# Kernel optimization log

Measured on AMD Instinct MI355X. Metric: run time of the kernel, lower is better.

Reference implementation:

```python
import jax, jax.numpy as jnp
import numpy as np

L, H, E, T, B, V = 8, 16, 1024, 1024, 2, 800
D = E // H  # head_size = 64
STD = 0.02


def setup_inputs() -> dict:
    key = jax.random.key(0)
    ks = iter(jax.random.split(key, 32))

    def nrm(shape):
        return jax.random.normal(next(ks), shape, jnp.float32) * STD

    latlong = jax.random.uniform(next(ks), (B, T, 2), jnp.float32)
    wl = jax.random.uniform(next(ks), (B, T, 1), jnp.float32, minval=3.0, maxval=11.0)
    inp = {
        "idx": jnp.concatenate([latlong, wl], axis=-1),  # [B,T,3]
        "tok_table": nrm((V, E)),
        "pos_W": nrm((2, E)),
        "pos_b": jnp.zeros((E,), jnp.float32),
        # stacked per-layer params (per-head q/k/v linears fused into [E,E])
        "Wq": nrm((L, E, E)),
        "Wk": nrm((L, E, E)),
        "Wv": nrm((L, E, E)),
        "Wo": nrm((L, E, E)),
        "bo": jnp.zeros((L, E), jnp.float32),
        "W1": nrm((L, E, 4 * E)),
        "b1": jnp.zeros((L, 4 * E), jnp.float32),
        "W2": nrm((L, 4 * E, E)),
        "b2": jnp.zeros((L, E), jnp.float32),
        "ln1_g": jnp.ones((L, E), jnp.float32),
        "ln1_b": jnp.zeros((L, E), jnp.float32),
        "ln2_g": jnp.ones((L, E), jnp.float32),
        "ln2_b": jnp.zeros((L, E), jnp.float32),
        "lnf_g": jnp.ones((E,), jnp.float32),
        "lnf_b": jnp.zeros((E,), jnp.float32),
        "lm_W": nrm((E, V)),
        "lm_b": jnp.zeros((V,), jnp.float32),
    }
    return inp


def _ln(x, g, b, eps=1e-5):
    m = x.mean(-1, keepdims=True)
    v = x.var(-1, keepdims=True)
    return (x - m) * jax.lax.rsqrt(v + eps) * g + b


def _block(x, p):
    Wq, Wk, Wv, Wo, bo, W1, b1, W2, b2, g1, be1, g2, be2 = p
    Bx, Tx, _ = x.shape
    h = _ln(x, g1, be1)
    q = (h @ Wq).reshape(Bx, Tx, H, D)
    k = (h @ Wk).reshape(Bx, Tx, H, D)
    v = (h @ Wv).reshape(Bx, Tx, H, D)
    scores = jnp.einsum('bqhd,bkhd->bhqk', q, k) * (D ** -0.5)
    mask = jnp.tril(jnp.ones((Tx, Tx), bool))  # causal
    scores = jnp.where(mask, scores, -jnp.inf)
    w = jax.nn.softmax(scores, axis=-1)  # dropout=0 (eval) -> identity
    attn = jnp.einsum('bhqk,bkhd->bqhd', w, v).reshape(Bx, Tx, E)
    x = x + attn @ Wo + bo
    h = _ln(x, g2, be2)
    x = x + jax.nn.relu(h @ W1 + b1) @ W2 + b2
    return x


def reference(idx, tok_table, pos_W, pos_b, Wq, Wk, Wv, Wo, bo, W1, b1, W2, b2,
              ln1_g, ln1_b, ln2_g, ln2_b, lnf_g, lnf_b, lm_W, lm_b):
    # water level channel -> token id in [0, V-1]
    idx_wl = jnp.clip(jnp.round(idx[..., 2] * 100.0 - 300.0), 0, V - 1).astype(jnp.int32)
    tok_emb = tok_table[idx_wl]                      # [B,T,E]
    pos_emb = idx[..., :2] @ pos_W + pos_b           # [B,T,E]
    x = tok_emb + pos_emb

    params = (Wq, Wk, Wv, Wo, bo, W1, b1, W2, b2, ln1_g, ln1_b, ln2_g, ln2_b)

    def body(carry, p):
        return _block(carry, p), None

    x, _ = jax.lax.scan(body, x, params)
    x = _ln(x, lnf_g, lnf_b)
    logits = x @ lm_W + lm_b                         # [B,T,V]
    return logits
```

## Files before the change

kernel.cpp:

```cpp
#include <hip/hip_runtime.h>
#include <hip/hip_bf16.h>

#define L_ 8
#define H_ 16
#define E_ 1024
#define T_ 1024
#define B_ 2
#define V_ 800
#define D_ 64
#define FF_ 4096
#define N_ (B_ * T_)
#define QS_ 3072

typedef unsigned short u16;
typedef __bf16 bf16x8 __attribute__((ext_vector_type(8)));
typedef float f32x4 __attribute__((ext_vector_type(4)));

__device__ __forceinline__ u16 f2b(float f) {
    unsigned int u = __float_as_uint(f);
    unsigned int r = (u + 0x7fffu + ((u >> 16) & 1u)) >> 16;
    return (u16)r;
}

__device__ __forceinline__ void gld16(const u16* g, u16* l) {
    __builtin_amdgcn_global_load_lds(
        (__attribute__((address_space(1))) void*)(uintptr_t)g,
        (__attribute__((address_space(3))) void*)(unsigned)(uintptr_t)l,
        16, 0, 0);
}

__global__ __launch_bounds__(256) void embed_k(
    const float* __restrict__ idx, const float* __restrict__ tok,
    const float* __restrict__ posW, const float* __restrict__ posb,
    float* __restrict__ x)
{
    int row = blockIdx.x;
    int e = threadIdx.x * 4;
    float lat = idx[row * 3 + 0];
    float lon = idx[row * 3 + 1];
    float wl  = idx[row * 3 + 2];
    float tf = rintf(wl * 100.0f - 300.0f);
    tf = fminf(fmaxf(tf, 0.0f), (float)(V_ - 1));
    int tkn = (int)tf;

    float4 tv = *(const float4*)(tok + (size_t)tkn * E_ + e);
    float4 p0 = *(const float4*)(posW + e);
    float4 p1 = *(const float4*)(posW + E_ + e);
    float4 pb = *(const float4*)(posb + e);
    float4 ov;
    ov.x = tv.x + lat * p0.x + lon * p1.x + pb.x;
    ov.y = tv.y + lat * p0.y + lon * p1.y + pb.y;
    ov.z = tv.z + lat * p0.z + lon * p1.z + pb.z;
    ov.w = tv.w + lat * p0.w + lon * p1.w + pb.w;
    *(float4*)(x + (size_t)row * E_ + e) = ov;
}

__global__ __launch_bounds__(256) void ln_k(
    const float* __restrict__ x, const float* __restrict__ g,
    const float* __restrict__ bta, u16* __restrict__ out)
{
    __shared__ float rs[4], rq[4];
    int row = blockIdx.x;
    int tid = threadIdx.x;
    const float* xr = x + (size_t)row * E_;
    float4 xv = *(const float4*)(xr + tid * 4);
    float s = xv.x + xv.y + xv.z + xv.w;
    float q = xv.x * xv.x + xv.y * xv.y + xv.z * xv.z + xv.w * xv.w;
    #pragma unroll
    for (int off = 32; off; off >>= 1) {
        s += __shfl_xor(s, off, 64);
        q += __shfl_xor(q, off, 64);
    }
    int wv = tid >> 6, ln = tid & 63;
    if (ln == 0) { rs[wv] = s; rq[wv] = q; }
    __syncthreads();
    s = rs[0] + rs[1] + rs[2] + rs[3];
    q = rq[0] + rq[1] + rq[2] + rq[3];
    float mean = s * (1.0f / E_);
    float var  = q * (1.0f / E_) - mean * mean;
    float inv  = 1.0f / sqrtf(var + 1e-5f);
    int c = tid * 4;
    float4 gv = *(const float4*)(g + c);
    float4 bv = *(const float4*)(bta + c);
    ushort4 ov;
    ov.x = f2b((xv.x - mean) * inv * gv.x + bv.x);
    ov.y = f2b((xv.y - mean) * inv * gv.y + bv.y);
    ov.z = f2b((xv.z - mean) * inv * gv.z + bv.z);
    ov.w = f2b((xv.w - mean) * inv * gv.w + bv.w);
    *(ushort4*)(out + (size_t)row * E_ + c) = ov;
}

__global__ __launch_bounds__(256) void comb_ln_k(
    const float* __restrict__ Cp, const float* __restrict__ bias,
    float* __restrict__ x, const float* __restrict__ g,
    const float* __restrict__ bta, u16* __restrict__ hout)
{
    __shared__ float rs[4], rq[4];
    int row = blockIdx.x;
    int tid = threadIdx.x;
    int c = tid * 4;
    size_t off = (size_t)row * E_ + c;
    const size_t total = (size_t)N_ * E_;
    float4 p0 = *(const float4*)(Cp + off);
    float4 p1 = *(const float4*)(Cp + total + off);
    float4 xv = *(const float4*)(x + off);
    float4 bv = *(const float4*)(bias + c);
    xv.x += p0.x + p1.x + bv.x;
    xv.y += p0.y + p1.y + bv.y;
    xv.z += p0.z + p1.z + bv.z;
    xv.w += p0.w + p1.w + bv.w;
    *(float4*)(x + off) = xv;

    float s = xv.x + xv.y + xv.z + xv.w;
    float q = xv.x * xv.x + xv.y * xv.y + xv.z * xv.z + xv.w * xv.w;
    #pragma unroll
    for (int o = 32; o; o >>= 1) {
        s += __shfl_xor(s, o, 64);
        q += __shfl_xor(q, o, 64);
    }
    int wv = tid >> 6, ln = tid & 63;
    if (ln == 0) { rs[wv] = s; rq[wv] = q; }
    __syncthreads();
    s = rs[0] + rs[1] + rs[2] + rs[3];
    q = rq[0] + rq[1] + rq[2] + rq[3];
    float mean = s * (1.0f / E_);
    float var  = q * (1.0f / E_) - mean * mean;
    float inv  = 1.0f / sqrtf(var + 1e-5f);
    float4 gv = *(const float4*)(g + c);
    float4 bb = *(const float4*)(bta + c);
    ushort4 ov;
    ov.x = f2b((xv.x - mean) * inv * gv.x + bb.x);
    ov.y = f2b((xv.y - mean) * inv * gv.y + bb.y);
    ov.z = f2b((xv.z - mean) * inv * gv.z + bb.z);
    ov.w = f2b((xv.w - mean) * inv * gv.w + bb.w);
    *(ushort4*)(hout + off) = ov;
}

__device__ __forceinline__ void wtrans_body(
    const float* __restrict__ W, u16* __restrict__ Wt, int K, int M,
    int m0, int k0)
{
    __shared__ float tile[64][65];
    int tid = threadIdx.x;
    int rr = tid >> 4, c4 = (tid & 15) * 4;
    if (m0 + 64 <= M) {
        #pragma unroll
        for (int p = 0; p < 4; p++) {
            int kk = rr + p * 16;
            float4 v4 = *(const float4*)(W + (size_t)(k0 + kk) * M + m0 + c4);
            tile[kk][c4 + 0] = v4.x; tile[kk][c4 + 1] = v4.y;
            tile[kk][c4 + 2] = v4.z; tile[kk][c4 + 3] = v4.w;
        }
    } else {
        #pragma unroll
        for (int p = 0; p < 4; p++) {
            int kk = rr + p * 16;
            const float* wr = W + (size_t)(k0 + kk) * M;
            #pragma unroll
            for (int c = 0; c < 4; c++) {
                int m = m0 + c4 + c;
                tile[kk][c4 + c] = (m < M) ? wr[m] : 0.0f;
            }
        }
    }
    __syncthreads();
    #pragma unroll
    for (int p = 0; p < 4; p++) {
        int ml = rr + p * 16;
        ushort4 o;
        o.x = f2b(tile[c4 + 0][ml]);
        o.y = f2b(tile[c4 + 1][ml]);
        o.z = f2b(tile[c4 + 2][ml]);
        o.w = f2b(tile[c4 + 3][ml]);
        *(ushort4*)(Wt + (size_t)(m0 + ml) * K + k0 + c4) = o;
    }
}

__global__ __launch_bounds__(256) void wtrans_k(
    const float* __restrict__ W, u16* __restrict__ Wt, int K, int M)
{
    wtrans_body(W, Wt, K, M, blockIdx.x * 64, blockIdx.y * 64);
}

__global__ __launch_bounds__(256) void wtrans_all_k(
    const float* __restrict__ Wq, const float* __restrict__ Wk,
    const float* __restrict__ Wv, const float* __restrict__ Wo,
    const float* __restrict__ W1, const float* __restrict__ W2,
    u16* __restrict__ wqkv_t, u16* __restrict__ wo_t,
    u16* __restrict__ w1_t, u16* __restrict__ w2_t)
{
    int bx = blockIdx.x, by = blockIdx.y, z = blockIdx.z;
    const size_t M1 = 1024 * 1024;
    if (z < 4) {
        if (bx >= 16) return;
        const float* W = (z == 0) ? Wq : (z == 1) ? Wk : (z == 2) ? Wv : Wo;
        u16* dst = (z < 3) ? (wqkv_t + (size_t)z * M1) : wo_t;
        wtrans_body(W, dst, E_, E_, bx * 64, by * 64);
    } else if (z == 4) {
        wtrans_body(W1, w1_t, E_, FF_, bx * 64, by * 64);
    } else {
        int id = by * 64 + bx;
        int mb = id >> 6, kb = id & 63;
        wtrans_body(W2, w2_t, FF_, E_, mb * 64, kb * 64);
    }
}

__global__ __launch_bounds__(256) void gemm_bf16(
    const u16* __restrict__ A, const u16* __restrict__ Bt,
    const float* __restrict__ bias, const float* __restrict__ res,
    float* __restrict__ Cf, u16* __restrict__ Cb, float* __restrict__ Cp,
    int K, int M, int relu)
{
    __shared__ __align__(16) u16 As[128 * 32];
    __shared__ __align__(16) u16 Bs[128 * 32];
    int tid = threadIdx.x;
    int bm = blockIdx.y * 128, bn = blockIdx.x * 128;
    int zz = blockIdx.z;
    int kslice = K / (int)gridDim.z;
    int lane = tid & 63, wv = tid >> 6;
    int l15 = lane & 15, q4 = lane >> 4;
    int wm = (wv & 1) * 64, wn = (wv >> 1) * 64;

    const u16* ga = A + (size_t)(bm + (tid >> 2)) * K + zz * kslice + (tid & 3) * 8;
    const u16* gb = Bt + (size_t)(bn + (tid >> 2)) * K + zz * kslice + (tid & 3) * 8;
    size_t gstep = (size_t)64 * K;
    u16* lA0 = As + wv * (16 * 32);
    u16* lB0 = Bs + wv * (16 * 32);

    f32x4 acc[4][4];
    #pragma unroll
    for (int i = 0; i < 4; i++)
        #pragma unroll
        for (int j = 0; j < 4; j++)
            acc[i][j] = (f32x4){0.0f, 0.0f, 0.0f, 0.0f};

    for (int k0 = 0; k0 < kslice; k0 += 32) {
        gld16(ga, lA0);
        gld16(ga + gstep, lA0 + 64 * 32);
        gld16(gb, lB0);
        gld16(gb + gstep, lB0 + 64 * 32);
        ga += 32; gb += 32;
        __syncthreads();

        const bf16x8* Ap = (const bf16x8*)As + (wm + l15) * 4 + q4;
        const bf16x8* Bp = (const bf16x8*)Bs + (wn + l15) * 4 + q4;
        bf16x8 af[4], bg[4];
        #pragma unroll
        for (int i = 0; i < 4; i++) { af[i] = Ap[i * 64]; bg[i] = Bp[i * 64]; }
        #pragma unroll
        for (int i = 0; i < 4; i++)
            #pragma unroll
            for (int j = 0; j < 4; j++)
                acc[i][j] = __builtin_amdgcn_mfma_f32_16x16x32_bf16(
                    af[i], bg[j], acc[i][j], 0, 0, 0);
        __syncthreads();
    }

    size_t poff = (size_t)zz * N_ * M;
    #pragma unroll
    for (int i = 0; i < 4; i++) {
        int r0 = bm + wm + i * 16 + q4 * 4;
        #pragma unroll
        for (int j = 0; j < 4; j++) {
            int col = bn + wn + j * 16 + l15;
            if (col < M) {
                if (Cp) {
                    #pragma unroll
                    for (int r = 0; r < 4; r++)
                        Cp[poff + (size_t)(r0 + r) * M + col] = acc[i][j][r];
                } else {
                    float bv = bias ? bias[col] : 0.0f;
                    #pragma unroll
                    for (int r = 0; r < 4; r++) {
                        size_t off = (size_t)(r0 + r) * M + col;
                        float v = acc[i][j][r] + bv;
                        if (res) v += res[off];
                        if (relu) v = fmaxf(v, 0.0f);
                        if (Cb) Cb[off] = f2b(v); else Cf[off] = v;
                    }
                }
            }
        }
    }
}

__global__ __launch_bounds__(256) void combine_k(
    const float* __restrict__ Cp, const float* __restrict__ bias,
    float* __restrict__ Cf, int M, int total)
{
    int e = (blockIdx.x * 256 + threadIdx.x) * 4;
    if (e >= total) return;
    float4 a = *(const float4*)(Cp + e);
    float4 b = *(const float4*)(Cp + (size_t)total + e);
    a.x += b.x; a.y += b.y; a.z += b.z; a.w += b.w;
    int col = e % M;
    if (bias) {
        float4 bv = *(const float4*)(bias + col);
        a.x += bv.x; a.y += bv.y; a.z += bv.z; a.w += bv.w;
    }
    *(float4*)(Cf + e) = a;
}

__global__ __launch_bounds__(256) void vtrans_k(
    const u16* __restrict__ QKV, u16* __restrict__ Vt)
{
    __shared__ u16 tile[64][72];
    int t0 = blockIdx.x * 64, h = blockIdx.y, b = blockIdx.z;
    int tid = threadIdx.x;
    int row = tid >> 3, c8 = (tid & 7) * 8;
    #pragma unroll
    for (int p = 0; p < 2; p++) {
        int t = row + p * 32;
        *(float4*)&tile[t][c8] = *(const float4*)(
            QKV + (size_t)(b * T_ + t0 + t) * QS_ + 2 * E_ + h * D_ + c8);
    }
    __syncthreads();
    #pragma unroll
    for (int p = 0; p < 2; p++) {
        int d = row + p * 32;
        u16 o[8];
        #pragma unroll
        for (int j = 0; j < 8; j++) o[j] = tile[c8 + j][d];
        *(ushort4*)(Vt + ((size_t)(b * H_ + h) * D_ + d) * T_ + t0 + c8) =
            *(ushort4*)&o[0];
        *(ushort4*)(Vt + ((size_t)(b * H_ + h) * D_ + d) * T_ + t0 + c8 + 4) =
            *(ushort4*)&o[4];
    }
}

__global__ __launch_bounds__(256) void attn_mfma_k(
    const u16* __restrict__ QKV, const u16* __restrict__ Vt,
    u16* __restrict__ O)
{
    __shared__ __align__(16) u16 Ps[4][16 * 72];
    int tid = threadIdx.x;
    int wv = tid >> 6, lane = tid & 63;
    int c = lane & 15, q4 = lane >> 4;
    int qb = (int)(gridDim.x - 1) - (int)blockIdx.x;
    int h = blockIdx.y, b = blockIdx.z;
    int q0 = qb * 64 + wv * 16;
    const float scale = 0.125f;

    const u16* qrow = QKV + (size_t)(b * T_ + q0 + c) * QS_ + h * D_;
    bf16x8 qf0 = *(const bf16x8*)(qrow + q4 * 8);
    bf16x8 qf1 = *(const bf16x8*)(qrow + 32 + q4 * 8);

    const u16* kbase  = QKV + (size_t)b * T_ * QS_ + E_ + h * D_;
    const u16* vtbase = Vt + (size_t)(b * H_ + h) * D_ * T_;

    float l_acc[4] = {0.0f, 0.0f, 0.0f, 0.0f};
    f32x4 acc_o[4];
    #pragma unroll
    for (int nt = 0; nt < 4; nt++) acc_o[nt] = (f32x4){0.f, 0.f, 0.f, 0.f};

    u16* ps = &Ps[wv][0];

    for (int kt = 0; kt <= qb; kt++) {
        int k0 = kt * 64;
        bool diag = (kt == qb);

        bf16x8 kf[4][2];
        #pragma unroll
        for (int j = 0; j < 4; j++) {
            const u16* kr = kbase + (size_t)(k0 + 16 * j + c) * QS_ + q4 * 8;
            kf[j][0] = *(const bf16x8*)(kr);
            kf[j][1] = *(const bf16x8*)(kr + 32);
        }

        #pragma unroll
        for (int j = 0; j < 4; j++) {
            f32x4 sa = (f32x4){0.f, 0.f, 0.f, 0.f};
            sa = __builtin_amdgcn_mfma_f32_16x16x32_bf16(qf0, kf[j][0], sa, 0, 0, 0);
            sa = __builtin_amdgcn_mfma_f32_16x16x32_bf16(qf1, kf[j][1], sa, 0, 0, 0);
            #pragma unroll
            for (int r = 0; r < 4; r++) {
                bool masked = diag && (k0 + 16 * j + c > q0 + 4 * q4 + r);
                float pj = masked ? 0.0f : __expf(sa[r] * scale);
                l_acc[r] += pj;
                ps[(4 * q4 + r) * 72 + 16 * j + c] = f2b(pj);
            }
        }
        bf16x8 pf0 = *(const bf16x8*)(ps + c * 72 + q4 * 8);
        bf16x8 pf1 = *(const bf16x8*)(ps + c * 72 + 32 + q4 * 8);

        bf16x8 vf[4][2];
        #pragma unroll
        for (int nt = 0; nt < 4; nt++) {
            const u16* vr = vtbase + (size_t)(16 * nt + c) * T_ + k0 + q4 * 8;
            vf[nt][0] = *(const bf16x8*)(vr);
            vf[nt][1] = *(const bf16x8*)(vr + 32);
        }

        #pragma unroll
        for (int nt = 0; nt < 4; nt++) {
            acc_o[nt] = __builtin_amdgcn_mfma_f32_16x16x32_bf16(pf0, vf[nt][0], acc_o[nt], 0, 0, 0);
            acc_o[nt] = __builtin_amdgcn_mfma_f32_16x16x32_bf16(pf1, vf[nt][1], acc_o[nt], 0, 0, 0);
        }
    }

    #pragma unroll
    for (int r = 0; r < 4; r++) {
        float ts = l_acc[r];
        ts += __shfl_xor(ts, 1, 64);
        ts += __shfl_xor(ts, 2, 64);
        ts += __shfl_xor(ts, 4, 64);
        ts += __shfl_xor(ts, 8, 64);
        l_acc[r] = ts;
    }

    #pragma unroll
    for (int r = 0; r < 4; r++) {
        float inv = 1.0f / l_acc[r];
        size_t orow = (size_t)(b * T_ + q0 + 4 * q4 + r) * E_ + h * D_;
        #pragma unroll
        for (int nt = 0; nt < 4; nt++)
            O[orow + 16 * nt + c] = f2b(acc_o[nt][r] * inv);
    }
}

extern "C" void kernel_launch(void* const* d_in, const int* in_sizes, int n_in,
                              void* d_out, int out_size, void* d_ws, size_t ws_size,
                              hipStream_t stream)
{
    const float* idx   = (const float*)d_in[0];
    const float* tok   = (const float*)d_in[1];
    const float* posW  = (const float*)d_in[2];
    const float* posb  = (const float*)d_in[3];
    const float* Wq    = (const float*)d_in[4];
    const float* Wk    = (const float*)d_in[5];
    const float* Wv    = (const float*)d_in[6];
    const float* Wo    = (const float*)d_in[7];
    const float* bo    = (const float*)d_in[8];
    const float* W1    = (const float*)d_in[9];
    const float* b1    = (const float*)d_in[10];
    const float* W2    = (const float*)d_in[11];
    const float* b2    = (const float*)d_in[12];
    const float* ln1g  = (const float*)d_in[13];
    const float* ln1b  = (const float*)d_in[14];
    const float* ln2g  = (const float*)d_in[15];
    const float* ln2b  = (const float*)d_in[16];
    const float* lnfg  = (const float*)d_in[17];
    const float* lnfb  = (const float*)d_in[18];
    const float* lmW   = (const float*)d_in[19];
    const float* lmb   = (const float*)d_in[20];
    float* out = (float*)d_out;

    const size_t M1 = 1024 * 1024;
    float* ws    = (float*)d_ws;
    float* x     = ws;
    float* cpart = x + 2 * M1;
    u16* qkv   = (u16*)(cpart + 4 * M1);
    u16* vt    = qkv + 6 * M1;
    u16* h_bf  = vt + 2 * M1;
    u16* ao_bf = h_bf + 2 * M1;
    u16* ff_bf = ao_bf + 2 * M1;
    u16* wq_t  = ff_bf + 8 * M1;
    u16* wo_t  = wq_t + 3 * M1;
    u16* w1_t  = wo_t + 1 * M1;
    u16* w2_t  = w1_t + 4 * M1;
    u16* wlm_t = w2_t + 4 * M1;

    dim3 blk(256);
    dim3 gQKV(3072 / 128, N_ / 128, 1);
    dim3 gWo(1024 / 128, N_ / 128, 2);
    dim3 gW1(4096 / 128, N_ / 128, 1);
    dim3 gW2(1024 / 128, N_ / 128, 2);
    dim3 gLM(7, N_ / 128, 2);
    dim3 gAT(T_ / 64, H_, B_);
    dim3 gWT(64, 16, 6);
    dim3 tLM(14, 16);
    int totLM = N_ * V_;
    dim3 cLM(totLM / 4 / 256);

    embed_k<<<N_, blk, 0, stream>>>(idx, tok, posW, posb, x);
    ln_k<<<N_, blk, 0, stream>>>(x, ln1g, ln1b, h_bf);

    for (int l = 0; l < L_; l++) {
        size_t oEE = (size_t)l * E_ * E_;
        size_t oE  = (size_t)l * E_;
        size_t oEF = (size_t)l * E_ * FF_;
        size_t oF  = (size_t)l * FF_;

        wtrans_all_k<<<gWT, blk, 0, stream>>>(
            Wq + oEE, Wk + oEE, Wv + oEE, Wo + oEE, W1 + oEF, W2 + oEF,
            wq_t, wo_t, w1_t, w2_t);
        gemm_bf16<<<gQKV, blk, 0, stream>>>(h_bf, wq_t, nullptr, nullptr,
                                            nullptr, qkv, nullptr, E_, QS_, 0);
        vtrans_k<<<gAT, blk, 0, stream>>>(qkv, vt);
        attn_mfma_k<<<gAT, blk, 0, stream>>>(qkv, vt, ao_bf);
        gemm_bf16<<<gWo, blk, 0, stream>>>(ao_bf, wo_t, nullptr, nullptr,
                                           nullptr, nullptr, cpart, E_, E_, 0);
        comb_ln_k<<<N_, blk, 0, stream>>>(cpart, bo + oE, x,
                                          ln2g + oE, ln2b + oE, h_bf);
        gemm_bf16<<<gW1, blk, 0, stream>>>(h_bf, w1_t, b1 + oF, nullptr,
                                           nullptr, ff_bf, nullptr, E_, FF_, 1);
        gemm_bf16<<<gW2, blk, 0, stream>>>(ff_bf, w2_t, nullptr, nullptr,
                                           nullptr, nullptr, cpart, FF_, E_, 0);
        if (l < L_ - 1) {
            comb_ln_k<<<N_, blk, 0, stream>>>(cpart, b2 + oE, x,
                                              ln1g + oE + E_, ln1b + oE + E_, h_bf);
        } else {
            comb_ln_k<<<N_, blk, 0, stream>>>(cpart, b2 + oE, x,
                                              lnfg, lnfb, h_bf);
        }
    }

    wtrans_k<<<tLM, blk, 0, stream>>>(lmW, wlm_t, E_, V_);
    gemm_bf16<<<gLM, blk, 0, stream>>>(h_bf, wlm_t, nullptr, nullptr,
                                       nullptr, nullptr, cpart, E_, V_, 0);
    combine_k<<<cLM, blk, 0, stream>>>(cpart, lmb, out, V_, totLM);
}
```

Before: 2.172 ms.

## Hoist weight transposes, fuse V-transpose into QKV GEMM, fuse embed+LN, deepen W2 split-K

```diff
diff --git a/kernel.cpp b/kernel.cpp
--- a/kernel.cpp
+++ b/kernel.cpp
@@ -29,13 +29,16 @@
         16, 0, 0);
 }
 
-__global__ __launch_bounds__(256) void embed_k(
+__global__ __launch_bounds__(256) void embed_ln_k(
     const float* __restrict__ idx, const float* __restrict__ tok,
     const float* __restrict__ posW, const float* __restrict__ posb,
-    float* __restrict__ x)
-{
+    const float* __restrict__ g, const float* __restrict__ bta,
+    float* __restrict__ x, u16* __restrict__ hout)
+{
+    __shared__ float rs[4], rq[4];
     int row = blockIdx.x;
-    int e = threadIdx.x * 4;
+    int tid = threadIdx.x;
+    int e = tid * 4;
     float lat = idx[row * 3 + 0];
     float lon = idx[row * 3 + 1];
     float wl  = idx[row * 3 + 2];
@@ -47,23 +50,13 @@
     float4 p0 = *(const float4*)(posW + e);
     float4 p1 = *(const float4*)(posW + E_ + e);
     float4 pb = *(const float4*)(posb + e);
-    float4 ov;
-    ov.x = tv.x + lat * p0.x + lon * p1.x + pb.x;
-    ov.y = tv.y + lat * p0.y + lon * p1.y + pb.y;
-    ov.z = tv.z + lat * p0.z + lon * p1.z + pb.z;
-    ov.w = tv.w + lat * p0.w + lon * p1.w + pb.w;
-    *(float4*)(x + (size_t)row * E_ + e) = ov;
-}
-
-__global__ __launch_bounds__(256) void ln_k(
-    const float* __restrict__ x, const float* __restrict__ g,
-    const float* __restrict__ bta, u16* __restrict__ out)
-{
-    __shared__ float rs[4], rq[4];
-    int row = blockIdx.x;
-    int tid = threadIdx.x;
-    const float* xr = x + (size_t)row * E_;
-    float4 xv = *(const float4*)(xr + tid * 4);
+    float4 xv;
+    xv.x = tv.x + lat * p0.x + lon * p1.x + pb.x;
+    xv.y = tv.y + lat * p0.y + lon * p1.y + pb.y;
+    xv.z = tv.z + lat * p0.z + lon * p1.z + pb.z;
+    xv.w = tv.w + lat * p0.w + lon * p1.w + pb.w;
+    *(float4*)(x + (size_t)row * E_ + e) = xv;
+
     float s = xv.x + xv.y + xv.z + xv.w;
     float q = xv.x * xv.x + xv.y * xv.y + xv.z * xv.z + xv.w * xv.w;
     #pragma unroll
@@ -79,19 +72,18 @@
     float mean = s * (1.0f / E_);
     float var  = q * (1.0f / E_) - mean * mean;
     float inv  = 1.0f / sqrtf(var + 1e-5f);
-    int c = tid * 4;
-    float4 gv = *(const float4*)(g + c);
-    float4 bv = *(const float4*)(bta + c);
+    float4 gv = *(const float4*)(g + e);
+    float4 bb = *(const float4*)(bta + e);
     ushort4 ov;
-    ov.x = f2b((xv.x - mean) * inv * gv.x + bv.x);
-    ov.y = f2b((xv.y - mean) * inv * gv.y + bv.y);
-    ov.z = f2b((xv.z - mean) * inv * gv.z + bv.z);
-    ov.w = f2b((xv.w - mean) * inv * gv.w + bv.w);
-    *(ushort4*)(out + (size_t)row * E_ + c) = ov;
+    ov.x = f2b((xv.x - mean) * inv * gv.x + bb.x);
+    ov.y = f2b((xv.y - mean) * inv * gv.y + bb.y);
+    ov.z = f2b((xv.z - mean) * inv * gv.z + bb.z);
+    ov.w = f2b((xv.w - mean) * inv * gv.w + bb.w);
+    *(ushort4*)(hout + (size_t)row * E_ + e) = ov;
 }
 
 __global__ __launch_bounds__(256) void comb_ln_k(
-    const float* __restrict__ Cp, const float* __restrict__ bias,
+    const float* __restrict__ Cp, int ns, const float* __restrict__ bias,
     float* __restrict__ x, const float* __restrict__ g,
     const float* __restrict__ bta, u16* __restrict__ hout)
 {
@@ -101,14 +93,13 @@
     int c = tid * 4;
     size_t off = (size_t)row * E_ + c;
     const size_t total = (size_t)N_ * E_;
-    float4 p0 = *(const float4*)(Cp + off);
-    float4 p1 = *(const float4*)(Cp + total + off);
     float4 xv = *(const float4*)(x + off);
     float4 bv = *(const float4*)(bias + c);
-    xv.x += p0.x + p1.x + bv.x;
-    xv.y += p0.y + p1.y + bv.y;
-    xv.z += p0.z + p1.z + bv.z;
-    xv.w += p0.w + p1.w + bv.w;
+    xv.x += bv.x; xv.y += bv.y; xv.z += bv.z; xv.w += bv.w;
+    for (int s2 = 0; s2 < ns; s2++) {
+        float4 p = *(const float4*)(Cp + (size_t)s2 * total + off);
+        xv.x += p.x; xv.y += p.y; xv.z += p.z; xv.w += p.w;
+    }
     *(float4*)(x + off) = xv;
 
     float s = xv.x + xv.y + xv.z + xv.w;
@@ -186,22 +177,50 @@
     const float* __restrict__ Wq, const float* __restrict__ Wk,
     const float* __restrict__ Wv, const float* __restrict__ Wo,
     const float* __restrict__ W1, const float* __restrict__ W2,
-    u16* __restrict__ wqkv_t, u16* __restrict__ wo_t,
-    u16* __restrict__ w1_t, u16* __restrict__ w2_t)
-{
+    u16* __restrict__ wt)
+{
+    const size_t MU = 1024 * 1024;
     int bx = blockIdx.x, by = blockIdx.y, z = blockIdx.z;
-    const size_t M1 = 1024 * 1024;
     if (z < 4) {
         if (bx >= 16) return;
         const float* W = (z == 0) ? Wq : (z == 1) ? Wk : (z == 2) ? Wv : Wo;
-        u16* dst = (z < 3) ? (wqkv_t + (size_t)z * M1) : wo_t;
-        wtrans_body(W, dst, E_, E_, bx * 64, by * 64);
+        wtrans_body(W, wt + (size_t)z * MU, E_, E_, bx * 64, by * 64);
     } else if (z == 4) {
-        wtrans_body(W1, w1_t, E_, FF_, bx * 64, by * 64);
+        wtrans_body(W1, wt + 4 * MU, E_, FF_, bx * 64, by * 64);
     } else {
         int id = by * 64 + bx;
-        int mb = id >> 6, kb = id & 63;
-        wtrans_body(W2, w2_t, FF_, E_, mb * 64, kb * 64);
+        wtrans_body(W2, wt + 8 * MU, FF_, E_, (id >> 6) * 64, (id & 63) * 64);
+    }
+}
+
+__global__ __launch_bounds__(256) void wtrans_hoist_k(
+    const float* __restrict__ Wq, const float* __restrict__ Wk,
+    const float* __restrict__ Wv, const float* __restrict__ Wo,
+    const float* __restrict__ W1, const float* __restrict__ W2,
+    const float* __restrict__ lmW,
+    u16* __restrict__ wslab, u16* __restrict__ wlm)
+{
+    const size_t MU = 1024 * 1024;
+    int bx = blockIdx.x, by = blockIdx.y, z = blockIdx.z;
+    if (z == 48) {
+        if (bx >= 14) return;
+        wtrans_body(lmW, wlm, E_, V_, bx * 64, by * 64);
+        return;
+    }
+    int l = z / 6, m = z % 6;
+    u16* wt = wslab + (size_t)l * 12 * MU;
+    size_t oEE = (size_t)l * E_ * E_;
+    size_t oEF = (size_t)l * E_ * FF_;
+    if (m < 4) {
+        if (bx >= 16) return;
+        const float* W = (m == 0) ? Wq + oEE : (m == 1) ? Wk + oEE
+                       : (m == 2) ? Wv + oEE : Wo + oEE;
+        wtrans_body(W, wt + (size_t)m * MU, E_, E_, bx * 64, by * 64);
+    } else if (m == 4) {
+        wtrans_body(W1 + oEF, wt + 4 * MU, E_, FF_, bx * 64, by * 64);
+    } else {
+        int id = by * 64 + bx;
+        wtrans_body(W2 + oEF, wt + 8 * MU, FF_, E_, (id >> 6) * 64, (id & 63) * 64);
     }
 }
 
@@ -209,7 +228,7 @@
     const u16* __restrict__ A, const u16* __restrict__ Bt,
     const float* __restrict__ bias, const float* __restrict__ res,
     float* __restrict__ Cf, u16* __restrict__ Cb, float* __restrict__ Cp,
-    int K, int M, int relu)
+    u16* __restrict__ vtout, int K, int M, int relu)
 {
     __shared__ __align__(16) u16 As[128 * 32];
     __shared__ __align__(16) u16 Bs[128 * 32];
@@ -276,7 +295,17 @@
                         float v = acc[i][j][r] + bv;
                         if (res) v += res[off];
                         if (relu) v = fmaxf(v, 0.0f);
-                        if (Cb) Cb[off] = f2b(v); else Cf[off] = v;
+                        if (vtout && col >= 2 * E_) {
+                            int dd = col - 2 * E_;
+                            int hh = dd >> 6, dl = dd & 63;
+                            int rowi = r0 + r;
+                            int bb = rowi >> 10, tt = rowi & 1023;
+                            vtout[((size_t)(bb * H_ + hh) * D_ + dl) * T_ + tt] = f2b(v);
+                        } else if (Cb) {
+                            Cb[off] = f2b(v);
+                        } else {
+                            Cf[off] = v;
+                        }
                     }
                 }
             }
@@ -299,33 +328,6 @@
         a.x += bv.x; a.y += bv.y; a.z += bv.z; a.w += bv.w;
     }
     *(float4*)(Cf + e) = a;
-}
-
-__global__ __launch_bounds__(256) void vtrans_k(
-    const u16* __restrict__ QKV, u16* __restrict__ Vt)
-{
-    __shared__ u16 tile[64][72];
-    int t0 = blockIdx.x * 64, h = blockIdx.y, b = blockIdx.z;
-    int tid = threadIdx.x;
-    int row = tid >> 3, c8 = (tid & 7) * 8;
-    #pragma unroll
-    for (int p = 0; p < 2; p++) {
-        int t = row + p * 32;
-        *(float4*)&tile[t][c8] = *(const float4*)(
-            QKV + (size_t)(b * T_ + t0 + t) * QS_ + 2 * E_ + h * D_ + c8);
-    }
-    __syncthreads();
-    #pragma unroll
-    for (int p = 0; p < 2; p++) {
-        int d = row + p * 32;
-        u16 o[8];
-        #pragma unroll
-        for (int j = 0; j < 8; j++) o[j] = tile[c8 + j][d];
-        *(ushort4*)(Vt + ((size_t)(b * H_ + h) * D_ + d) * T_ + t0 + c8) =
-            *(ushort4*)&o[0];
-        *(ushort4*)(Vt + ((size_t)(b * H_ + h) * D_ + d) * T_ + t0 + c8 + 4) =
-            *(ushort4*)&o[4];
-    }
 }
 
 __global__ __launch_bounds__(256) void attn_mfma_k(
@@ -445,35 +447,45 @@
     const float* lmb   = (const float*)d_in[20];
     float* out = (float*)d_out;
 
-    const size_t M1 = 1024 * 1024;
+    const size_t MU = 1024ull * 1024ull;
+    size_t need_big = (2 + 8) * MU * 4
+                    + (6 + 2 + 2 + 8) * MU * 2
+                    + (8 * 12 * MU + 896 * 1024) * 2;
+    bool big = ws_size >= need_big;
+    size_t ncp = big ? 8 * MU : 4 * MU;
+    int w2z = big ? 4 : 2;
+
     float* ws    = (float*)d_ws;
     float* x     = ws;
-    float* cpart = x + 2 * M1;
-    u16* qkv   = (u16*)(cpart + 4 * M1);
-    u16* vt    = qkv + 6 * M1;
-    u16* h_bf  = vt + 2 * M1;
-    u16* ao_bf = h_bf + 2 * M1;
-    u16* ff_bf = ao_bf + 2 * M1;
-    u16* wq_t  = ff_bf + 8 * M1;
-    u16* wo_t  = wq_t + 3 * M1;
-    u16* w1_t  = wo_t + 1 * M1;
-    u16* w2_t  = w1_t + 4 * M1;
-    u16* wlm_t = w2_t + 4 * M1;
+    float* cpart = x + 2 * MU;
+    u16* qkv   = (u16*)(cpart + ncp);
+    u16* vt    = qkv + 6 * MU;
+    u16* h_bf  = vt + 2 * MU;
+    u16* ff_bf = h_bf + 2 * MU;
+    u16* wslab = ff_bf + 8 * MU;
+    u16* wlm   = big ? (wslab + 8 * 12 * MU) : (wslab + 12 * MU);
 
     dim3 blk(256);
     dim3 gQKV(3072 / 128, N_ / 128, 1);
     dim3 gWo(1024 / 128, N_ / 128, 2);
     dim3 gW1(4096 / 128, N_ / 128, 1);
-    dim3 gW2(1024 / 128, N_ / 128, 2);
+    dim3 gW2(1024 / 128, N_ / 128, w2z);
     dim3 gLM(7, N_ / 128, 2);
     dim3 gAT(T_ / 64, H_, B_);
+    dim3 gHOIST(64, 16, 49);
     dim3 gWT(64, 16, 6);
     dim3 tLM(14, 16);
     int totLM = N_ * V_;
     dim3 cLM(totLM / 4 / 256);
 
-    embed_k<<<N_, blk, 0, stream>>>(idx, tok, posW, posb, x);
-    ln_k<<<N_, blk, 0, stream>>>(x, ln1g, ln1b, h_bf);
+    if (big) {
+        wtrans_hoist_k<<<gHOIST, blk, 0, stream>>>(
+            Wq, Wk, Wv, Wo, W1, W2, lmW, wslab, wlm);
+    } else {
+        wtrans_k<<<tLM, blk, 0, stream>>>(lmW, wlm, E_, V_);
+    }
+
+    embed_ln_k<<<N_, blk, 0, stream>>>(idx, tok, posW, posb, ln1g, ln1b, x, h_bf);
 
     for (int l = 0; l < L_; l++) {
         size_t oEE = (size_t)l * E_ * E_;
@@ -481,32 +493,42 @@
         size_t oEF = (size_t)l * E_ * FF_;
         size_t oF  = (size_t)l * FF_;
 
-        wtrans_all_k<<<gWT, blk, 0, stream>>>(
-            Wq + oEE, Wk + oEE, Wv + oEE, Wo + oEE, W1 + oEF, W2 + oEF,
-            wq_t, wo_t, w1_t, w2_t);
-        gemm_bf16<<<gQKV, blk, 0, stream>>>(h_bf, wq_t, nullptr, nullptr,
-                                            nullptr, qkv, nullptr, E_, QS_, 0);
-        vtrans_k<<<gAT, blk, 0, stream>>>(qkv, vt);
-        attn_mfma_k<<<gAT, blk, 0, stream>>>(qkv, vt, ao_bf);
-        gemm_bf16<<<gWo, blk, 0, stream>>>(ao_bf, wo_t, nullptr, nullptr,
-                                           nullptr, nullptr, cpart, E_, E_, 0);
-        comb_ln_k<<<N_, blk, 0, stream>>>(cpart, bo + oE, x,
+        u16* wt = big ? (wslab + (size_t)l * 12 * MU) : wslab;
+        if (!big) {
+            wtrans_all_k<<<gWT, blk, 0, stream>>>(
+                Wq + oEE, Wk + oEE, Wv + oEE, Wo + oEE, W1 + oEF, W2 + oEF, wt);
+        }
+        u16* wqkv_l = wt;
+        u16* wo_l   = wt + 3 * MU;
+        u16* w1_l   = wt + 4 * MU;
+        u16* w2_l   = wt + 8 * MU;
+
+        gemm_bf16<<<gQKV, blk, 0, stream>>>(h_bf, wqkv_l, nullptr, nullptr,
+                                            nullptr, qkv, nullptr, vt,
+                                            E_, QS_, 0);
+        attn_mfma_k<<<gAT, blk, 0, stream>>>(qkv, vt, h_bf );
+        gemm_bf16<<<gWo, blk, 0, stream>>>(h_bf, wo_l, nullptr, nullptr,
+                                           nullptr, nullptr, cpart, nullptr,
+                                           E_, E_, 0);
+        comb_ln_k<<<N_, blk, 0, stream>>>(cpart, 2, bo + oE, x,
                                           ln2g + oE, ln2b + oE, h_bf);
-        gemm_bf16<<<gW1, blk, 0, stream>>>(h_bf, w1_t, b1 + oF, nullptr,
-                                           nullptr, ff_bf, nullptr, E_, FF_, 1);
-        gemm_bf16<<<gW2, blk, 0, stream>>>(ff_bf, w2_t, nullptr, nullptr,
-                                           nullptr, nullptr, cpart, FF_, E_, 0);
+        gemm_bf16<<<gW1, blk, 0, stream>>>(h_bf, w1_l, b1 + oF, nullptr,
+                                           nullptr, ff_bf, nullptr, nullptr,
+                                           E_, FF_, 1);
+        gemm_bf16<<<gW2, blk, 0, stream>>>(ff_bf, w2_l, nullptr, nullptr,
+                                           nullptr, nullptr, cpart, nullptr,
+                                           FF_, E_, 0);
         if (l < L_ - 1) {
-            comb_ln_k<<<N_, blk, 0, stream>>>(cpart, b2 + oE, x,
+            comb_ln_k<<<N_, blk, 0, stream>>>(cpart, w2z, b2 + oE, x,
                                               ln1g + oE + E_, ln1b + oE + E_, h_bf);
         } else {
-            comb_ln_k<<<N_, blk, 0, stream>>>(cpart, b2 + oE, x,
+            comb_ln_k<<<N_, blk, 0, stream>>>(cpart, w2z, b2 + oE, x,
                                               lnfg, lnfb, h_bf);
         }
     }
 
-    wtrans_k<<<tLM, blk, 0, stream>>>(lmW, wlm_t, E_, V_);
-    gemm_bf16<<<gLM, blk, 0, stream>>>(h_bf, wlm_t, nullptr, nullptr,
-                                       nullptr, nullptr, cpart, E_, V_, 0);
+    gemm_bf16<<<gLM, blk, 0, stream>>>(h_bf, wlm, nullptr, nullptr,
+                                       nullptr, nullptr, cpart, nullptr,
+                                       E_, V_, 0);
     combine_k<<<cLM, blk, 0, stream>>>(cpart, lmb, out, V_, totLM);
 }
```

Result: no change. 2.179 ms (+0.3%).
